# Kernel optimization log

Hardware: AMD Instinct MI355X
Metric: run time of the kernel (lower is better)

Reference implementation:

```python
import jax, jax.numpy as jnp
import numpy as np

N, E, EMB, EDGE, ITERS = 50000, 400000, 128, 32, 2
EPS = 1e-5


def setup_inputs() -> dict:
    key = jax.random.key(0)
    ks = jax.random.split(key, 8)
    s = 0.05

    def lin(k, i, o):
        return jax.random.normal(k, (i, o), jnp.float32) * s

    def mlp_params(k):
        k1, k2 = jax.random.split(k)
        return dict(W1=lin(k1, 2 * EMB + EDGE, EMB), b1=jnp.zeros((EMB,)),
                    g1=jnp.ones((EMB,)), be1=jnp.zeros((EMB,)),
                    W2=lin(k2, EMB, EMB), b2=jnp.zeros((EMB,)),
                    g2=jnp.ones((EMB,)), be2=jnp.zeros((EMB,)))

    p = mlp_params(ks[3])
    c = mlp_params(ks[4])
    inp = {
        'nodes': jax.random.normal(ks[0], (N, EMB), jnp.float32),
        'edges': jax.random.randint(ks[1], (2, E), 0, N, jnp.int64),
        'edge_attr': jax.random.normal(ks[2], (E, EDGE), jnp.float32),
        'fW': lin(ks[5], EMB, EMB), 'fb': jnp.zeros((EMB,)),
        'fg': jnp.ones((EMB,)), 'fbe': jnp.zeros((EMB,)),
    }
    for name, d in (('p', p), ('c', c)):
        for kk, v in d.items():
            inp[name + kk] = v
    return inp


def _bn(x, g, b):
    # training-mode BatchNorm1d: batch stats over axis 0, biased variance
    m = x.mean(0)
    v = x.var(0)
    return (x - m) * jax.lax.rsqrt(v + EPS) * g + b


def _edge_mlp(h, W1, b1, g1, be1, W2, b2, g2, be2):
    h = jax.nn.relu(_bn(h @ W1 + b1, g1, be1))
    return jax.nn.relu(_bn(h @ W2 + b2, g2, be2))


def _agg(x, idx_i, idx_j, ea, params):
    # message: mlp([x_i, x_j, edge_attr]); aggregate sum at idx_i; degree-normalize
    msg = _edge_mlp(jnp.concatenate([x[idx_i], x[idx_j], ea], axis=1), *params)
    summed = jax.ops.segment_sum(msg, idx_i, num_segments=x.shape[0])
    deg = jax.ops.segment_sum(jnp.ones(idx_i.shape, x.dtype), idx_i,
                              num_segments=x.shape[0])
    deg_inv = jnp.where(deg > 0, 1.0 / deg, 0.0)
    return summed * deg_inv[:, None]


def reference(nodes, edges, edge_attr,
              pW1, pb1, pg1, pbe1, pW2, pb2, pg2, pbe2,
              cW1, cb1, cg1, cbe1, cW2, cb2, cg2, cbe2,
              fW, fb, fg, fbe):
    src, dst = edges[0], edges[1]
    pp = (pW1, pb1, pg1, pbe1, pW2, pb2, pg2, pbe2)
    cp = (cW1, cb1, cg1, cbe1, cW2, cb2, cg2, cbe2)
    for _ in range(ITERS):
        fi = _agg(nodes, dst, src, edge_attr, pp)  # parent: source_to_target
        fo = _agg(nodes, src, dst, edge_attr, cp)  # child: target_to_source
        upd = jax.nn.relu(_bn((nodes + fi + fo) @ fW + fb, fg, fbe))
        nodes = nodes + upd
    return nodes
```

## Files before the change

kernel.cpp:

```cpp
#include <hip/hip_runtime.h>
#include <math.h>

#define NN 50000
#define EE 400000
#define EMBD 128
#define KIN 288
#define NITERS 2
#define EPSV 1e-5f
#define SAE 296
#define SA1 136
#define NT_E 6250
#define G0 1024
#define G1 1024

typedef __attribute__((ext_vector_type(8))) short bf16x8;
typedef __attribute__((ext_vector_type(4))) float f32x4;

#define MFMA16(a, b, c) __builtin_amdgcn_mfma_f32_16x16x32_bf16(a, b, c, 0, 0, 0)

__device__ __forceinline__ unsigned short f2bf(float x) {
  unsigned int u = __float_as_uint(x);
  u += 0x7fffu + ((u >> 16) & 1u);
  return (unsigned short)(u >> 16);
}

__device__ __forceinline__ int physch(int ch, int row) {
  return (ch < 32) ? ((ch & ~7) | ((ch ^ (row & 7)) & 7)) : ch;
}


__global__ void k_zeroi(int* __restrict__ p, int n) {
  for (int i = blockIdx.x * blockDim.x + threadIdx.x; i < n;
       i += gridDim.x * blockDim.x)
    p[i] = 0;
}

__global__ void k_detect(const long long* __restrict__ e64, int* __restrict__ flag) {
  __shared__ int ok;
  if (threadIdx.x == 0) ok = 1;
  __syncthreads();
  for (int i = threadIdx.x; i < 4096; i += blockDim.x) {
    const long long v = e64[i];
    if (v < 0 || v >= NN) atomicAnd(&ok, 0);
  }
  __syncthreads();
  if (threadIdx.x == 0) *flag = ok;
}

__global__ void k_convert(const void* __restrict__ edges, const int* __restrict__ flag,
                          int* __restrict__ src, int* __restrict__ dst) {
  const int is64 = *flag;
  for (int i = blockIdx.x * blockDim.x + threadIdx.x; i < 2 * EE;
       i += gridDim.x * blockDim.x) {
    const int v = is64 ? (int)((const long long*)edges)[i] : ((const int*)edges)[i];
    if (i < EE) src[i] = v; else dst[i - EE] = v;
  }
}

__global__ void k_count(const int* __restrict__ src, const int* __restrict__ dst,
                        int* __restrict__ degp, int* __restrict__ degc) {
  for (int e = blockIdx.x * blockDim.x + threadIdx.x; e < EE;
       e += gridDim.x * blockDim.x) {
    atomicAdd(&degp[dst[e]], 1);
    atomicAdd(&degc[src[e]], 1);
  }
}

__global__ void k_dinv(const int* __restrict__ dp, const int* __restrict__ dc,
                       float* __restrict__ ip, float* __restrict__ ic) {
  for (int n = blockIdx.x * blockDim.x + threadIdx.x; n < NN;
       n += gridDim.x * blockDim.x) {
    ip[n] = dp[n] ? 1.f / (float)dp[n] : 0.f;
    ic[n] = dc[n] ? 1.f / (float)dc[n] : 0.f;
  }
}

__global__ __launch_bounds__(1024) void k_scan(
    const int* __restrict__ degp, const int* __restrict__ degc,
    int* __restrict__ offp, int* __restrict__ offc) {
  const int* deg = blockIdx.x ? degc : degp;
  int* off = blockIdx.x ? offc : offp;
  __shared__ int sh[1024];
  const int t = threadIdx.x;
  int running = 0;
  for (int base = 0; base < NN; base += 1024) {
    const int v = (base + t < NN) ? deg[base + t] : 0;
    sh[t] = v;
    __syncthreads();
    for (int o = 1; o < 1024; o <<= 1) {
      const int y = (t >= o) ? sh[t - o] : 0;
      __syncthreads();
      sh[t] += y;
      __syncthreads();
    }
    if (base + t < NN) off[base + t] = running + sh[t] - v;
    running += sh[1023];
    __syncthreads();
  }
  if (t == 0) off[NN] = running;
}

__global__ void k_copycur(const int* __restrict__ offp, const int* __restrict__ offc,
                          int* __restrict__ curp, int* __restrict__ curc) {
  for (int i = blockIdx.x * blockDim.x + threadIdx.x; i < NN;
       i += gridDim.x * blockDim.x) {
    curp[i] = offp[i];
    curc[i] = offc[i];
  }
}

__global__ void k_scatter(const int* __restrict__ src, const int* __restrict__ dst,
                          int* __restrict__ curp, int* __restrict__ curc,
                          int* __restrict__ lstp, int* __restrict__ lstc) {
  for (int e = blockIdx.x * blockDim.x + threadIdx.x; e < EE;
       e += gridDim.x * blockDim.x) {
    const int pp = atomicAdd(&curp[dst[e]], 1);
    lstp[pp] = e;
    const int pc = atomicAdd(&curc[src[e]], 1);
    lstc[pc] = e;
  }
}

__global__ void k_initnodes(const float* __restrict__ in, float* __restrict__ nd,
                            unsigned short* __restrict__ xb) {
  const int tot = NN * EMBD / 4;
  for (int i = blockIdx.x * blockDim.x + threadIdx.x; i < tot;
       i += gridDim.x * blockDim.x) {
    const float4 v = ((const float4*)in)[i];
    ((float4*)nd)[i] = v;
    short4 b;
    b.x = (short)f2bf(v.x); b.y = (short)f2bf(v.y);
    b.z = (short)f2bf(v.z); b.w = (short)f2bf(v.w);
    *(short4*)&xb[(size_t)i * 4] = b;
  }
}

__global__ void k_prepW(const float* __restrict__ W, unsigned short* __restrict__ Wt,
                        int K) {
  const int idx = blockIdx.x * blockDim.x + threadIdx.x;
  if (idx < K * EMBD) {
    const int k = idx >> 7, n = idx & 127;
    Wt[(size_t)n * K + k] = f2bf(W[(size_t)k * EMBD + n]);
  }
}

__global__ void k_prepea(const float* __restrict__ ea,
                         unsigned short* __restrict__ eab) {
  const int tot = EE * 32 / 8;
  for (int i = blockIdx.x * blockDim.x + threadIdx.x; i < tot;
       i += gridDim.x * blockDim.x) {
    const float4 a = ((const float4*)ea)[i * 2];
    const float4 b = ((const float4*)ea)[i * 2 + 1];
    union { unsigned short u[8]; uint4 v; } o;
    o.u[0] = f2bf(a.x); o.u[1] = f2bf(a.y); o.u[2] = f2bf(a.z); o.u[3] = f2bf(a.w);
    o.u[4] = f2bf(b.x); o.u[5] = f2bf(b.y); o.u[6] = f2bf(b.z); o.u[7] = f2bf(b.w);
    ((uint4*)eab)[i] = o.v;
  }
}


template <int EAB>
__global__ __launch_bounds__(256, 1) void k_pass0(
    const unsigned short* __restrict__ xb, const int* __restrict__ idx_i,
    const int* __restrict__ idx_j, const float* __restrict__ ea,
    const unsigned short* __restrict__ eab,
    const unsigned short* __restrict__ W1t, float* __restrict__ stat,
    unsigned short* __restrict__ Y1) {
  __shared__ __align__(16) unsigned short Ab[64 * SAE];
  __shared__ float red[256];
  const int t = threadIdx.x;
  const int lane = t & 63, w = t >> 6, m = lane & 15, kg = lane >> 4;
  const int r = t >> 2, sub = t & 3;
  const int n0 = w * 32 + m, n1 = n0 + 16;
  bf16x8 B0[9], B1[9];
#pragma unroll
  for (int ks = 0; ks < 9; ++ks) {
    B0[ks] = *(const bf16x8*)&W1t[(size_t)n0 * KIN + ks * 32 + kg * 8];
    B1[ks] = *(const bf16x8*)&W1t[(size_t)n1 * KIN + ks * 32 + kg * 8];
  }
  float s0 = 0.f, s1 = 0.f, q0 = 0.f, q1 = 0.f;
  int tile = blockIdx.x;
  int inext = idx_i[tile * 64 + r];
  int jnext = idx_j[tile * 64 + r];
  while (tile < NT_E) {
    const int icur = inext, jcur = jnext;
    __syncthreads();
    {
      const uint4* xi = (const uint4*)(xb + (size_t)icur * EMBD);
      const uint4* xj = (const uint4*)(xb + (size_t)jcur * EMBD);
      unsigned short* rowp = &Ab[r * SAE];
#pragma unroll
      for (int qq = 0; qq < 8; ++qq) {
        const int c = sub + qq * 4;
        const uint4 v = (c < 16) ? xi[c] : xj[c - 16];
        *(uint4*)&rowp[physch(c, r) * 8] = v;
      }
      const int e = tile * 64 + r;
      uint4 ev;
      if (EAB) {
        ev = *(const uint4*)&eab[(size_t)e * 32 + sub * 8];
      } else {
        const float4 e0 = *(const float4*)&ea[(size_t)e * 32 + sub * 8];
        const float4 e1 = *(const float4*)&ea[(size_t)e * 32 + sub * 8 + 4];
        union { unsigned short u[8]; uint4 v4; } o;
        o.u[0] = f2bf(e0.x); o.u[1] = f2bf(e0.y); o.u[2] = f2bf(e0.z);
        o.u[3] = f2bf(e0.w); o.u[4] = f2bf(e1.x); o.u[5] = f2bf(e1.y);
        o.u[6] = f2bf(e1.z); o.u[7] = f2bf(e1.w);
        ev = o.v4;
      }
      *(uint4*)&rowp[(32 + sub) * 8] = ev;
    }
    __syncthreads();
    const int next = tile + gridDim.x;
    if (next < NT_E) {
      inext = idx_i[next * 64 + r];
      jnext = idx_j[next * 64 + r];
    }
    const f32x4 zz = {0.f, 0.f, 0.f, 0.f};
    f32x4 acc[4][2] = {{zz, zz}, {zz, zz}, {zz, zz}, {zz, zz}};
#pragma unroll
    for (int ks = 0; ks < 9; ++ks) {
      const int aoff = physch(ks * 4 + kg, m) * 8;
#pragma unroll
      for (int mt = 0; mt < 4; ++mt) {
        const bf16x8 a = *(const bf16x8*)&Ab[(mt * 16 + m) * SAE + aoff];
        acc[mt][0] = MFMA16(a, B0[ks], acc[mt][0]);
        acc[mt][1] = MFMA16(a, B1[ks], acc[mt][1]);
      }
    }
#pragma unroll
    for (int mt = 0; mt < 4; ++mt)
#pragma unroll
      for (int r2 = 0; r2 < 4; ++r2) {
        const float v0 = acc[mt][0][r2], v1 = acc[mt][1][r2];
        s0 += v0; q0 += v0 * v0;
        s1 += v1; q1 += v1 * v1;
      }
    __syncthreads();
#pragma unroll
    for (int nt = 0; nt < 2; ++nt) {
      const int c = w * 32 + nt * 16 + m;
      const int cc = c >> 3, cl = c & 7;
#pragma unroll
      for (int mt = 0; mt < 4; ++mt)
#pragma unroll
        for (int r2 = 0; r2 < 4; ++r2) {
          const int rw = mt * 16 + kg * 4 + r2;
          Ab[rw * SAE + physch(cc, rw) * 8 + cl] = f2bf(acc[mt][nt][r2]);
        }
    }
    __syncthreads();
    unsigned short* Yt = Y1 + (size_t)tile * 64 * EMBD;
#pragma unroll
    for (int i = 0; i < 4; ++i) {
      const int g = i * 2048 + t * 8;
      const int row = g >> 7, ch = (g >> 3) & 15;
      *(uint4*)&Yt[g] = *(const uint4*)&Ab[row * SAE + physch(ch, row) * 8];
    }
    tile = next;
  }
  s0 += __shfl_xor(s0, 16); s0 += __shfl_xor(s0, 32);
  q0 += __shfl_xor(q0, 16); q0 += __shfl_xor(q0, 32);
  s1 += __shfl_xor(s1, 16); s1 += __shfl_xor(s1, 32);
  q1 += __shfl_xor(q1, 16); q1 += __shfl_xor(q1, 32);
  if (kg == 0) {
    const int c0 = w * 32 + m, c1 = c0 + 16;
    red[c0] = s0; red[128 + c0] = q0;
    red[c1] = s1; red[128 + c1] = q1;
  }
  __syncthreads();
  if (t < 128) {
    atomicAdd(&stat[t], red[t]);
    atomicAdd(&stat[128 + t], red[128 + t]);
  }
}


__global__ __launch_bounds__(256, 3) void k_pass1(
    const unsigned short* __restrict__ W2t, float* __restrict__ stat,
    unsigned short* __restrict__ Y) {
  __shared__ __align__(16) unsigned short Ab[64 * SA1];
  __shared__ float red[256];
  const int t = threadIdx.x;
  const int lane = t & 63, w = t >> 6, m = lane & 15, kg = lane >> 4;
  const int n0 = w * 32 + m, n1 = n0 + 16;
  const int ch = t & 15;
  bf16x8 B0[4], B1[4];
#pragma unroll
  for (int ks = 0; ks < 4; ++ks) {
    B0[ks] = *(const bf16x8*)&W2t[(size_t)n0 * EMBD + ks * 32 + kg * 8];
    B1[ks] = *(const bf16x8*)&W2t[(size_t)n1 * EMBD + ks * 32 + kg * 8];
  }
  float scr[8], shr[8];
#pragma unroll
  for (int h = 0; h < 8; ++h) {
    scr[h] = stat[256 + ch * 8 + h];
    shr[h] = stat[384 + ch * 8 + h];
  }
  float s0 = 0.f, s1 = 0.f, q0 = 0.f, q1 = 0.f;
  uint4 yreg[4];
  int tile = blockIdx.x;
  {
    const unsigned short* Yt = Y + (size_t)tile * 64 * EMBD;
#pragma unroll
    for (int i = 0; i < 4; ++i)
      yreg[i] = *(const uint4*)&Yt[i * 2048 + t * 8];
  }
  while (tile < NT_E) {
    __syncthreads();
#pragma unroll
    for (int i = 0; i < 4; ++i) {
      const int row = i * 16 + (t >> 4);
      const unsigned int* pv = (const unsigned int*)&yreg[i];
      union { unsigned short u[8]; uint4 v; } o;
#pragma unroll
      for (int h = 0; h < 4; ++h) {
        const unsigned int pw = pv[h];
        const float f0 = __uint_as_float(pw << 16);
        const float f1 = __uint_as_float(pw & 0xffff0000u);
        o.u[h * 2] = f2bf(fmaxf(fmaf(f0, scr[h * 2], shr[h * 2]), 0.f));
        o.u[h * 2 + 1] = f2bf(fmaxf(fmaf(f1, scr[h * 2 + 1], shr[h * 2 + 1]), 0.f));
      }
      *(uint4*)&Ab[row * SA1 + physch(ch, row) * 8] = o.v;
    }
    __syncthreads();
    const int next = tile + gridDim.x;
    if (next < NT_E) {
      const unsigned short* Yt = Y + (size_t)next * 64 * EMBD;
#pragma unroll
      for (int i = 0; i < 4; ++i)
        yreg[i] = *(const uint4*)&Yt[i * 2048 + t * 8];
    }
    const f32x4 zz = {0.f, 0.f, 0.f, 0.f};
    f32x4 acc[4][2] = {{zz, zz}, {zz, zz}, {zz, zz}, {zz, zz}};
#pragma unroll
    for (int ks = 0; ks < 4; ++ks) {
      const int aoff = physch(ks * 4 + kg, m) * 8;
#pragma unroll
      for (int mt = 0; mt < 4; ++mt) {
        const bf16x8 a = *(const bf16x8*)&Ab[(mt * 16 + m) * SA1 + aoff];
        acc[mt][0] = MFMA16(a, B0[ks], acc[mt][0]);
        acc[mt][1] = MFMA16(a, B1[ks], acc[mt][1]);
      }
    }
#pragma unroll
    for (int mt = 0; mt < 4; ++mt)
#pragma unroll
      for (int r2 = 0; r2 < 4; ++r2) {
        const float v0 = acc[mt][0][r2], v1 = acc[mt][1][r2];
        s0 += v0; q0 += v0 * v0;
        s1 += v1; q1 += v1 * v1;
      }
    __syncthreads();
#pragma unroll
    for (int nt = 0; nt < 2; ++nt) {
      const int c = w * 32 + nt * 16 + m;
      const int cc = c >> 3, cl = c & 7;
#pragma unroll
      for (int mt = 0; mt < 4; ++mt)
#pragma unroll
        for (int r2 = 0; r2 < 4; ++r2) {
          const int rw = mt * 16 + kg * 4 + r2;
          Ab[rw * SA1 + physch(cc, rw) * 8 + cl] = f2bf(acc[mt][nt][r2]);
        }
    }
    __syncthreads();
    unsigned short* Yo = Y + (size_t)tile * 64 * EMBD;
#pragma unroll
    for (int i = 0; i < 4; ++i) {
      const int g = i * 2048 + t * 8;
      const int row = g >> 7, c2 = (g >> 3) & 15;
      *(uint4*)&Yo[g] = *(const uint4*)&Ab[row * SA1 + physch(c2, row) * 8];
    }
    tile = next;
  }
  s0 += __shfl_xor(s0, 16); s0 += __shfl_xor(s0, 32);
  q0 += __shfl_xor(q0, 16); q0 += __shfl_xor(q0, 32);
  s1 += __shfl_xor(s1, 16); s1 += __shfl_xor(s1, 32);
  q1 += __shfl_xor(q1, 16); q1 += __shfl_xor(q1, 32);
  if (kg == 0) {
    const int c0 = w * 32 + m, c1 = c0 + 16;
    red[c0] = s0; red[128 + c0] = q0;
    red[c1] = s1; red[128 + c1] = q1;
  }
  __syncthreads();
  if (t < 128) {
    atomicAdd(&stat[512 + t], red[t]);
    atomicAdd(&stat[640 + t], red[128 + t]);
  }
}


template <int ADD>
__global__ __launch_bounds__(256) void k_agg2(
    const unsigned short* __restrict__ Y2, const int* __restrict__ off,
    const int* __restrict__ lst, const float* __restrict__ stat,
    const float* __restrict__ dinv, float* __restrict__ agg) {
  const int n = blockIdx.x * 4 + (threadIdx.x >> 6);
  const int lane = threadIdx.x & 63;
  if (n >= NN) return;
  const int o0 = off[n], o1 = off[n + 1];
  const float sc0 = stat[768 + 2 * lane], sc1 = stat[768 + 2 * lane + 1];
  const float sh0 = stat[896 + 2 * lane], sh1 = stat[896 + 2 * lane + 1];
  float a0 = 0.f, a1 = 0.f;
  for (int o = o0; o < o1; ++o) {
    const int e = lst[o];
    const unsigned int pw = ((const unsigned int*)(Y2 + (size_t)e * EMBD))[lane];
    a0 += fmaxf(fmaf(__uint_as_float(pw << 16), sc0, sh0), 0.f);
    a1 += fmaxf(fmaf(__uint_as_float(pw & 0xffff0000u), sc1, sh1), 0.f);
  }
  const float d = dinv[n];
  float2 out;
  if (ADD) {
    const float2 prev = ((const float2*)(agg + (size_t)n * EMBD))[lane];
    out.x = prev.x + a0 * d;
    out.y = prev.y + a1 * d;
  } else {
    out.x = a0 * d;
    out.y = a1 * d;
  }
  ((float2*)(agg + (size_t)n * EMBD))[lane] = out;
}


template <int NK, bool SWZ>
__device__ __forceinline__ void gemm_g(const unsigned short* Ab, const int sa,
                                       const unsigned short* __restrict__ Wt,
                                       const int K, const int m, const int kg,
                                       const int w, f32x4 acc[4][2]) {
  const int n0 = w * 32 + m, n1 = n0 + 16;
#pragma unroll
  for (int ks = 0; ks < NK; ++ks) {
    const int koff = ks * 32 + kg * 8;
    const int aoff = SWZ ? physch(koff >> 3, m) * 8 : koff;
    const bf16x8 b0 = *(const bf16x8*)&Wt[(size_t)n0 * K + koff];
    const bf16x8 b1 = *(const bf16x8*)&Wt[(size_t)n1 * K + koff];
#pragma unroll
    for (int mt = 0; mt < 4; ++mt) {
      const bf16x8 a = *(const bf16x8*)&Ab[(mt * 16 + m) * sa + aoff];
      acc[mt][0] = MFMA16(a, b0, acc[mt][0]);
      acc[mt][1] = MFMA16(a, b1, acc[mt][1]);
    }
  }
}

__device__ __forceinline__ void stats_epi64(const f32x4 acc[4][2], float* red,
                                            float* __restrict__ statg, const int t,
                                            const int m, const int kg, const int w) {
#pragma unroll
  for (int nt = 0; nt < 2; ++nt) {
    float s = 0.f, q = 0.f;
#pragma unroll
    for (int mt = 0; mt < 4; ++mt)
#pragma unroll
      for (int r = 0; r < 4; ++r) {
        const float v = acc[mt][nt][r];
        s += v;
        q += v * v;
      }
    s += __shfl_xor(s, 16); s += __shfl_xor(s, 32);
    q += __shfl_xor(q, 16); q += __shfl_xor(q, 32);
    if (kg == 0) {
      const int c = w * 32 + nt * 16 + m;
      red[c] = s;
      red[128 + c] = q;
    }
  }
  __syncthreads();
  if (t < 128) {
    atomicAdd(&statg[t], red[t]);
    atomicAdd(&statg[128 + t], red[128 + t]);
  }
}

__global__ __launch_bounds__(256) void k_node(
    const float* __restrict__ nd, float* __restrict__ ag,
    const unsigned short* __restrict__ Wt, float* __restrict__ stat) {
  __shared__ __align__(16) unsigned short Ab[64 * SA1];
  __shared__ float red[256];
  const int t = threadIdx.x;
  const int n0 = blockIdx.x * 64;
  {
    const int r = t >> 2, sub = t & 3;
    const int row = n0 + r;
    unsigned short* drow = &Ab[r * SA1];
#pragma unroll
    for (int q = 0; q < 8; ++q) {
      const int c4 = sub + q * 4;
      float4 va;
      if (row < NN) {
        va = ((const float4*)(nd + (size_t)row * EMBD))[c4];
        const float4 vb = ((const float4*)(ag + (size_t)row * EMBD))[c4];
        va.x += vb.x; va.y += vb.y; va.z += vb.z; va.w += vb.w;
      } else {
        va.x = va.y = va.z = va.w = 0.f;
      }
      short4 b;
      b.x = (short)f2bf(va.x); b.y = (short)f2bf(va.y);
      b.z = (short)f2bf(va.z); b.w = (short)f2bf(va.w);
      *(short4*)&drow[c4 * 4] = b;
    }
  }
  __syncthreads();
  const int lane = t & 63, w = t >> 6, m = lane & 15, kg = lane >> 4;
  const f32x4 zz = {0.f, 0.f, 0.f, 0.f};
  f32x4 acc[4][2] = {{zz, zz}, {zz, zz}, {zz, zz}, {zz, zz}};
  gemm_g<4, false>(Ab, SA1, Wt, EMBD, m, kg, w, acc);
#pragma unroll
  for (int nt = 0; nt < 2; ++nt) {
    const int c = w * 32 + nt * 16 + m;
#pragma unroll
    for (int mt = 0; mt < 4; ++mt)
#pragma unroll
      for (int r = 0; r < 4; ++r) {
        const int row = n0 + mt * 16 + kg * 4 + r;
        if (row < NN) ag[(size_t)row * EMBD + c] = acc[mt][nt][r];
      }
  }
  stats_epi64(acc, red, stat, t, m, kg, w);
}


__global__ void k_finalize(float* __restrict__ statbase, const float* __restrict__ g,
                           const float* __restrict__ be, float cnt) {
  const int t = threadIdx.x;
  if (t < EMBD) {
    const float s = statbase[t], sq = statbase[EMBD + t];
    const float m = s / cnt;
    float v = sq / cnt - m * m;
    v = fmaxf(v, 0.f);
    const float rs = rsqrtf(v + EPSV);
    const float sc = g[t] * rs;
    statbase[256 + t] = sc;
    statbase[384 + t] = be[t] - m * sc;
    statbase[t] = 0.f;
    statbase[EMBD + t] = 0.f;
  }
}

__global__ void k_update(float* __restrict__ nd, unsigned short* __restrict__ xb,
                         const float* __restrict__ Z, const float* __restrict__ stat) {
  const float* sc = stat + 256;
  const float* sh = stat + 384;
  const int total = NN * EMBD / 4;
  for (int i = blockIdx.x * blockDim.x + threadIdx.x; i < total;
       i += gridDim.x * blockDim.x) {
    const int c4 = i & 31;
    const float4 v = ((const float4*)Z)[i];
    const float4 s4 = ((const float4*)sc)[c4];
    const float4 h4 = ((const float4*)sh)[c4];
    float4 nv = ((float4*)nd)[i];
    nv.x += fmaxf(fmaf(v.x, s4.x, h4.x), 0.f);
    nv.y += fmaxf(fmaf(v.y, s4.y, h4.y), 0.f);
    nv.z += fmaxf(fmaf(v.z, s4.z, h4.z), 0.f);
    nv.w += fmaxf(fmaf(v.w, s4.w, h4.w), 0.f);
    ((float4*)nd)[i] = nv;
    short4 b;
    b.x = (short)f2bf(nv.x); b.y = (short)f2bf(nv.y);
    b.z = (short)f2bf(nv.z); b.w = (short)f2bf(nv.w);
    *(short4*)&xb[(size_t)i * 4] = b;
  }
}


extern "C" void kernel_launch(void* const* d_in, const int* in_sizes, int n_in,
                              void* d_out, int out_size, void* d_ws, size_t ws_size,
                              hipStream_t stream) {
  const float* in_nodes = (const float*)d_in[0];
  const void* edges = d_in[1];
  const float* ea = (const float*)d_in[2];
  const float* fW = (const float*)d_in[3];
  const float* fg = (const float*)d_in[5];
  const float* fbe = (const float*)d_in[6];
  const float* p_[8];
  const float* c_[8];
  for (int i = 0; i < 8; ++i) {
    p_[i] = (const float*)d_in[7 + i];
    c_[i] = (const float*)d_in[15 + i];
  }
  float* nodes = (float*)d_out;

  char* base = (char*)d_ws;
  size_t cur = 0;
  auto take = [&](size_t bytes) -> void* {
    void* p = base + cur;
    cur = (cur + bytes + 255) & ~(size_t)255;
    return p;
  };
  float* agg = (float*)take((size_t)NN * EMBD * 4);
  unsigned short* xb = (unsigned short*)take((size_t)NN * EMBD * 2);
  int* src = (int*)take(EE * 4);
  int* dst = (int*)take(EE * 4);
  int* lstp = (int*)take(EE * 4);
  int* lstc = (int*)take(EE * 4);
  int* offp = (int*)take((NN + 1) * 4);
  int* offc = (int*)take((NN + 1) * 4);
  int* curp = (int*)take(NN * 4);
  int* curc = (int*)take(NN * 4);
  float* dinvp = (float*)take(NN * 4);
  float* dinvc = (float*)take(NN * 4);
  float* stat = (float*)take(1024 * 4);
  int* flag = (int*)take(4);
  unsigned short* pW1t = (unsigned short*)take((size_t)EMBD * KIN * 2);
  unsigned short* pW2t = (unsigned short*)take((size_t)EMBD * EMBD * 2);
  unsigned short* cW1t = (unsigned short*)take((size_t)EMBD * KIN * 2);
  unsigned short* cW2t = (unsigned short*)take((size_t)EMBD * EMBD * 2);
  unsigned short* fWt = (unsigned short*)take((size_t)EMBD * EMBD * 2);
  unsigned short* Y1 = (unsigned short*)take((size_t)EE * EMBD * 2);
  const size_t eab_bytes = (size_t)EE * 32 * 2;
  const bool useEab = (cur + eab_bytes) <= ws_size;
  unsigned short* eab = useEab ? (unsigned short*)take(eab_bytes) : nullptr;

  k_zeroi<<<64, 256, 0, stream>>>((int*)stat, 1024);
  k_zeroi<<<128, 256, 0, stream>>>(curp, NN);
  k_zeroi<<<128, 256, 0, stream>>>(curc, NN);
  k_detect<<<1, 256, 0, stream>>>((const long long*)edges, flag);
  k_convert<<<1024, 256, 0, stream>>>(edges, flag, src, dst);
  k_count<<<1024, 256, 0, stream>>>(src, dst, curp, curc);
  k_dinv<<<128, 256, 0, stream>>>(curp, curc, dinvp, dinvc);
  k_scan<<<2, 1024, 0, stream>>>(curp, curc, offp, offc);
  k_copycur<<<128, 256, 0, stream>>>(offp, offc, curp, curc);
  k_scatter<<<1024, 256, 0, stream>>>(src, dst, curp, curc, lstp, lstc);
  k_initnodes<<<2048, 256, 0, stream>>>(in_nodes, nodes, xb);
  k_prepW<<<(KIN * EMBD + 255) / 256, 256, 0, stream>>>(p_[0], pW1t, KIN);
  k_prepW<<<(EMBD * EMBD + 255) / 256, 256, 0, stream>>>(p_[4], pW2t, EMBD);
  k_prepW<<<(KIN * EMBD + 255) / 256, 256, 0, stream>>>(c_[0], cW1t, KIN);
  k_prepW<<<(EMBD * EMBD + 255) / 256, 256, 0, stream>>>(c_[4], cW2t, EMBD);
  k_prepW<<<(EMBD * EMBD + 255) / 256, 256, 0, stream>>>(fW, fWt, EMBD);
  if (useEab) k_prepea<<<2048, 256, 0, stream>>>(ea, eab);

  const int NB = (NN + 63) / 64;

  for (int it = 0; it < NITERS; ++it) {
    if (useEab)
      k_pass0<1><<<G0, 256, 0, stream>>>(xb, dst, src, ea, eab, pW1t, stat, Y1);
    else
      k_pass0<0><<<G0, 256, 0, stream>>>(xb, dst, src, ea, eab, pW1t, stat, Y1);
    k_finalize<<<1, 128, 0, stream>>>(stat, p_[2], p_[3], (float)EE);
    k_pass1<<<G1, 256, 0, stream>>>(pW2t, stat, Y1);
    k_finalize<<<1, 128, 0, stream>>>(stat + 512, p_[6], p_[7], (float)EE);
    k_agg2<0><<<NN / 4, 256, 0, stream>>>(Y1, offp, lstp, stat, dinvp, agg);
    if (useEab)
      k_pass0<1><<<G0, 256, 0, stream>>>(xb, src, dst, ea, eab, cW1t, stat, Y1);
    else
      k_pass0<0><<<G0, 256, 0, stream>>>(xb, src, dst, ea, eab, cW1t, stat, Y1);
    k_finalize<<<1, 128, 0, stream>>>(stat, c_[2], c_[3], (float)EE);
    k_pass1<<<G1, 256, 0, stream>>>(cW2t, stat, Y1);
    k_finalize<<<1, 128, 0, stream>>>(stat + 512, c_[6], c_[7], (float)EE);
    k_agg2<1><<<NN / 4, 256, 0, stream>>>(Y1, offc, lstc, stat, dinvc, agg);
    k_node<<<NB, 256, 0, stream>>>(nodes, agg, fWt, stat);
    k_finalize<<<1, 128, 0, stream>>>(stat, fg, fbe, (float)NN);
    k_update<<<2048, 256, 0, stream>>>(nodes, xb, agg, stat);
  }
}
```

Before: 1.061 ms.

## Fuse parent and child first-layer edge GEMMs into one pass sharing gathered inputs

Adds a fused pass0 kernel that gathers [x_dst, x_src, ea] once per edge tile and computes both the parent and child first-layer GEMMs. The child weights are pre-permuted by swapping the first two 128-row K blocks, so the same gathered tile serves the reversed concatenation. This halves the random node gathers and tile staging, at the cost of a second edge-sized intermediate buffer, twice the resident weight registers and separate stat buffers. It also replaces the serial chunked degree scan with a per-thread-chunk scan using a single block-level prefix pass.

```diff
diff --git a/kernel.cpp b/kernel.cpp
--- a/kernel.cpp
+++ b/kernel.cpp
@@ -75,29 +75,38 @@
   }
 }
 
-__global__ __launch_bounds__(1024) void k_scan(
+__global__ __launch_bounds__(1024) void k_scan2(
     const int* __restrict__ degp, const int* __restrict__ degc,
     int* __restrict__ offp, int* __restrict__ offc) {
   const int* deg = blockIdx.x ? degc : degp;
   int* off = blockIdx.x ? offc : offp;
   __shared__ int sh[1024];
   const int t = threadIdx.x;
-  int running = 0;
-  for (int base = 0; base < NN; base += 1024) {
-    const int v = (base + t < NN) ? deg[base + t] : 0;
-    sh[t] = v;
-    __syncthreads();
-    for (int o = 1; o < 1024; o <<= 1) {
-      const int y = (t >= o) ? sh[t - o] : 0;
-      __syncthreads();
-      sh[t] += y;
-      __syncthreads();
-    }
-    if (base + t < NN) off[base + t] = running + sh[t] - v;
-    running += sh[1023];
-    __syncthreads();
-  }
-  if (t == 0) off[NN] = running;
+  const int i0 = t * 49;
+  int s = 0;
+#pragma unroll 1
+  for (int k = 0; k < 49; ++k) {
+    const int i = i0 + k;
+    if (i < NN) s += deg[i];
+  }
+  sh[t] = s;
+  __syncthreads();
+  for (int o = 1; o < 1024; o <<= 1) {
+    const int y = (t >= o) ? sh[t - o] : 0;
+    __syncthreads();
+    sh[t] += y;
+    __syncthreads();
+  }
+  int base = sh[t] - s;
+#pragma unroll 1
+  for (int k = 0; k < 49; ++k) {
+    const int i = i0 + k;
+    if (i < NN) {
+      off[i] = base;
+      base += deg[i];
+    }
+  }
+  if (t == 1023) off[NN] = sh[1023];
 }
 
 __global__ void k_copycur(const int* __restrict__ offp, const int* __restrict__ offc,
@@ -136,11 +145,12 @@
 }
 
 __global__ void k_prepW(const float* __restrict__ W, unsigned short* __restrict__ Wt,
-                        int K) {
+                        int K, int swap) {
   const int idx = blockIdx.x * blockDim.x + threadIdx.x;
   if (idx < K * EMBD) {
     const int k = idx >> 7, n = idx & 127;
-    Wt[(size_t)n * K + k] = f2bf(W[(size_t)k * EMBD + n]);
+    const int ksw = (swap && k < 256) ? (k ^ 128) : k;
+    Wt[(size_t)n * K + ksw] = f2bf(W[(size_t)k * EMBD + n]);
   }
 }
 
@@ -155,6 +165,142 @@
     o.u[0] = f2bf(a.x); o.u[1] = f2bf(a.y); o.u[2] = f2bf(a.z); o.u[3] = f2bf(a.w);
     o.u[4] = f2bf(b.x); o.u[5] = f2bf(b.y); o.u[6] = f2bf(b.z); o.u[7] = f2bf(b.w);
     ((uint4*)eab)[i] = o.v;
+  }
+}
+
+
+template <int EAB>
+__global__ __launch_bounds__(256, 1) void k_pass0f(
+    const unsigned short* __restrict__ xb, const int* __restrict__ idx_i,
+    const int* __restrict__ idx_j, const float* __restrict__ ea,
+    const unsigned short* __restrict__ eab,
+    const unsigned short* __restrict__ Wp, const unsigned short* __restrict__ Wc,
+    float* __restrict__ statP, float* __restrict__ statC,
+    unsigned short* __restrict__ Yp, unsigned short* __restrict__ Yc) {
+  __shared__ __align__(16) unsigned short Ab[64 * SAE];
+  __shared__ float red[512];
+  const int t = threadIdx.x;
+  const int lane = t & 63, w = t >> 6, m = lane & 15, kg = lane >> 4;
+  const int r = t >> 2, sub = t & 3;
+  const int n0 = w * 32 + m, n1 = n0 + 16;
+  bf16x8 Bp0[9], Bp1[9], Bc0[9], Bc1[9];
+#pragma unroll
+  for (int ks = 0; ks < 9; ++ks) {
+    Bp0[ks] = *(const bf16x8*)&Wp[(size_t)n0 * KIN + ks * 32 + kg * 8];
+    Bp1[ks] = *(const bf16x8*)&Wp[(size_t)n1 * KIN + ks * 32 + kg * 8];
+    Bc0[ks] = *(const bf16x8*)&Wc[(size_t)n0 * KIN + ks * 32 + kg * 8];
+    Bc1[ks] = *(const bf16x8*)&Wc[(size_t)n1 * KIN + ks * 32 + kg * 8];
+  }
+  float ps0 = 0.f, ps1 = 0.f, pq0 = 0.f, pq1 = 0.f;
+  float cs0 = 0.f, cs1 = 0.f, cq0 = 0.f, cq1 = 0.f;
+  int tile = blockIdx.x;
+  int inext = idx_i[tile * 64 + r];
+  int jnext = idx_j[tile * 64 + r];
+  while (tile < NT_E) {
+    const int icur = inext, jcur = jnext;
+    __syncthreads();
+    {
+      const uint4* xi = (const uint4*)(xb + (size_t)icur * EMBD);
+      const uint4* xj = (const uint4*)(xb + (size_t)jcur * EMBD);
+      unsigned short* rowp = &Ab[r * SAE];
+#pragma unroll
+      for (int qq = 0; qq < 8; ++qq) {
+        const int c = sub + qq * 4;
+        const uint4 v = (c < 16) ? xi[c] : xj[c - 16];
+        *(uint4*)&rowp[physch(c, r) * 8] = v;
+      }
+      const int e = tile * 64 + r;
+      uint4 ev;
+      if (EAB) {
+        ev = *(const uint4*)&eab[(size_t)e * 32 + sub * 8];
+      } else {
+        const float4 e0 = *(const float4*)&ea[(size_t)e * 32 + sub * 8];
+        const float4 e1 = *(const float4*)&ea[(size_t)e * 32 + sub * 8 + 4];
+        union { unsigned short u[8]; uint4 v4; } o;
+        o.u[0] = f2bf(e0.x); o.u[1] = f2bf(e0.y); o.u[2] = f2bf(e0.z);
+        o.u[3] = f2bf(e0.w); o.u[4] = f2bf(e1.x); o.u[5] = f2bf(e1.y);
+        o.u[6] = f2bf(e1.z); o.u[7] = f2bf(e1.w);
+        ev = o.v4;
+      }
+      *(uint4*)&rowp[(32 + sub) * 8] = ev;
+    }
+    __syncthreads();
+    const int next = tile + gridDim.x;
+    if (next < NT_E) {
+      inext = idx_i[next * 64 + r];
+      jnext = idx_j[next * 64 + r];
+    }
+    const f32x4 zz = {0.f, 0.f, 0.f, 0.f};
+    f32x4 ap[4][2] = {{zz, zz}, {zz, zz}, {zz, zz}, {zz, zz}};
+    f32x4 ac[4][2] = {{zz, zz}, {zz, zz}, {zz, zz}, {zz, zz}};
+#pragma unroll
+    for (int ks = 0; ks < 9; ++ks) {
+      const int aoff = physch(ks * 4 + kg, m) * 8;
+#pragma unroll
+      for (int mt = 0; mt < 4; ++mt) {
+        const bf16x8 a = *(const bf16x8*)&Ab[(mt * 16 + m) * SAE + aoff];
+        ap[mt][0] = MFMA16(a, Bp0[ks], ap[mt][0]);
+        ap[mt][1] = MFMA16(a, Bp1[ks], ap[mt][1]);
+        ac[mt][0] = MFMA16(a, Bc0[ks], ac[mt][0]);
+        ac[mt][1] = MFMA16(a, Bc1[ks], ac[mt][1]);
+      }
+    }
+#pragma unroll
+    for (int mt = 0; mt < 4; ++mt)
+#pragma unroll
+      for (int r2 = 0; r2 < 4; ++r2) {
+        const float p0 = ap[mt][0][r2], p1 = ap[mt][1][r2];
+        ps0 += p0; pq0 += p0 * p0; ps1 += p1; pq1 += p1 * p1;
+        const float c0 = ac[mt][0][r2], c1 = ac[mt][1][r2];
+        cs0 += c0; cq0 += c0 * c0; cs1 += c1; cq1 += c1 * c1;
+      }
+    __syncthreads();
+#pragma unroll
+    for (int nt = 0; nt < 2; ++nt) {
+      const int c = w * 32 + nt * 16 + m;
+      const int cc = c >> 3, cl = c & 7;
+#pragma unroll
+      for (int mt = 0; mt < 4; ++mt)
+#pragma unroll
+        for (int r2 = 0; r2 < 4; ++r2) {
+          const int rw = mt * 16 + kg * 4 + r2;
+          Ab[rw * SAE + physch(cc, rw) * 8 + cl] = f2bf(ap[mt][nt][r2]);
+          Ab[rw * SAE + physch(16 + cc, rw) * 8 + cl] = f2bf(ac[mt][nt][r2]);
+        }
+    }
+    __syncthreads();
+    unsigned short* Ytp = Yp + (size_t)tile * 64 * EMBD;
+    unsigned short* Ytc = Yc + (size_t)tile * 64 * EMBD;
+#pragma unroll
+    for (int i = 0; i < 4; ++i) {
+      const int g = i * 2048 + t * 8;
+      const int row = g >> 7, ch = (g >> 3) & 15;
+      *(uint4*)&Ytp[g] = *(const uint4*)&Ab[row * SAE + physch(ch, row) * 8];
+      *(uint4*)&Ytc[g] = *(const uint4*)&Ab[row * SAE + physch(ch + 16, row) * 8];
+    }
+    tile = next;
+  }
+  ps0 += __shfl_xor(ps0, 16); ps0 += __shfl_xor(ps0, 32);
+  pq0 += __shfl_xor(pq0, 16); pq0 += __shfl_xor(pq0, 32);
+  ps1 += __shfl_xor(ps1, 16); ps1 += __shfl_xor(ps1, 32);
+  pq1 += __shfl_xor(pq1, 16); pq1 += __shfl_xor(pq1, 32);
+  cs0 += __shfl_xor(cs0, 16); cs0 += __shfl_xor(cs0, 32);
+  cq0 += __shfl_xor(cq0, 16); cq0 += __shfl_xor(cq0, 32);
+  cs1 += __shfl_xor(cs1, 16); cs1 += __shfl_xor(cs1, 32);
+  cq1 += __shfl_xor(cq1, 16); cq1 += __shfl_xor(cq1, 32);
+  if (kg == 0) {
+    const int c0 = w * 32 + m, c1 = c0 + 16;
+    red[c0] = ps0; red[128 + c0] = pq0;
+    red[c1] = ps1; red[128 + c1] = pq1;
+    red[256 + c0] = cs0; red[384 + c0] = cq0;
+    red[256 + c1] = cs1; red[384 + c1] = cq1;
+  }
+  __syncthreads();
+  if (t < 128) {
+    atomicAdd(&statP[t], red[t]);
+    atomicAdd(&statP[128 + t], red[128 + t]);
+    atomicAdd(&statC[t], red[256 + t]);
+    atomicAdd(&statC[128 + t], red[384 + t]);
   }
 }
 
@@ -599,57 +745,81 @@
   int* curc = (int*)take(NN * 4);
   float* dinvp = (float*)take(NN * 4);
   float* dinvc = (float*)take(NN * 4);
-  float* stat = (float*)take(1024 * 4);
+  float* stat = (float*)take(2048 * 4);
   int* flag = (int*)take(4);
   unsigned short* pW1t = (unsigned short*)take((size_t)EMBD * KIN * 2);
   unsigned short* pW2t = (unsigned short*)take((size_t)EMBD * EMBD * 2);
   unsigned short* cW1t = (unsigned short*)take((size_t)EMBD * KIN * 2);
+  unsigned short* cW1ts = (unsigned short*)take((size_t)EMBD * KIN * 2);
   unsigned short* cW2t = (unsigned short*)take((size_t)EMBD * EMBD * 2);
   unsigned short* fWt = (unsigned short*)take((size_t)EMBD * EMBD * 2);
-  unsigned short* Y1 = (unsigned short*)take((size_t)EE * EMBD * 2);
+  unsigned short* Y1p = (unsigned short*)take((size_t)EE * EMBD * 2);
+  const size_t y_bytes = (size_t)EE * EMBD * 2;
+  const bool useF = (cur + y_bytes) <= ws_size;
+  unsigned short* Y1c = useF ? (unsigned short*)take(y_bytes) : nullptr;
   const size_t eab_bytes = (size_t)EE * 32 * 2;
   const bool useEab = (cur + eab_bytes) <= ws_size;
   unsigned short* eab = useEab ? (unsigned short*)take(eab_bytes) : nullptr;
 
-  k_zeroi<<<64, 256, 0, stream>>>((int*)stat, 1024);
+  k_zeroi<<<64, 256, 0, stream>>>((int*)stat, 2048);
   k_zeroi<<<128, 256, 0, stream>>>(curp, NN);
   k_zeroi<<<128, 256, 0, stream>>>(curc, NN);
   k_detect<<<1, 256, 0, stream>>>((const long long*)edges, flag);
   k_convert<<<1024, 256, 0, stream>>>(edges, flag, src, dst);
   k_count<<<1024, 256, 0, stream>>>(src, dst, curp, curc);
   k_dinv<<<128, 256, 0, stream>>>(curp, curc, dinvp, dinvc);
-  k_scan<<<2, 1024, 0, stream>>>(curp, curc, offp, offc);
+  k_scan2<<<2, 1024, 0, stream>>>(curp, curc, offp, offc);
   k_copycur<<<128, 256, 0, stream>>>(offp, offc, curp, curc);
   k_scatter<<<1024, 256, 0, stream>>>(src, dst, curp, curc, lstp, lstc);
   k_initnodes<<<2048, 256, 0, stream>>>(in_nodes, nodes, xb);
-  k_prepW<<<(KIN * EMBD + 255) / 256, 256, 0, stream>>>(p_[0], pW1t, KIN);
-  k_prepW<<<(EMBD * EMBD + 255) / 256, 256, 0, stream>>>(p_[4], pW2t, EMBD);
-  k_prepW<<<(KIN * EMBD + 255) / 256, 256, 0, stream>>>(c_[0], cW1t, KIN);
-  k_prepW<<<(EMBD * EMBD + 255) / 256, 256, 0, stream>>>(c_[4], cW2t, EMBD);
-  k_prepW<<<(EMBD * EMBD + 255) / 256, 256, 0, stream>>>(fW, fWt, EMBD);
+  k_prepW<<<(KIN * EMBD + 255) / 256, 256, 0, stream>>>(p_[0], pW1t, KIN, 0);
+  k_prepW<<<(EMBD * EMBD + 255) / 256, 256, 0, stream>>>(p_[4], pW2t, EMBD, 0);
+  k_prepW<<<(KIN * EMBD + 255) / 256, 256, 0, stream>>>(c_[0], cW1t, KIN, 0);
+  k_prepW<<<(KIN * EMBD + 255) / 256, 256, 0, stream>>>(c_[0], cW1ts, KIN, 1);
+  k_prepW<<<(EMBD * EMBD + 255) / 256, 256, 0, stream>>>(c_[4], cW2t, EMBD, 0);
+  k_prepW<<<(EMBD * EMBD + 255) / 256, 256, 0, stream>>>(fW, fWt, EMBD, 0);
   if (useEab) k_prepea<<<2048, 256, 0, stream>>>(ea, eab);
 
   const int NB = (NN + 63) / 64;
+  float* statP = stat;
+  float* statC = stat + 1024;
 
   for (int it = 0; it < NITERS; ++it) {
-    if (useEab)
-      k_pass0<1><<<G0, 256, 0, stream>>>(xb, dst, src, ea, eab, pW1t, stat, Y1);
-    else
-      k_pass0<0><<<G0, 256, 0, stream>>>(xb, dst, src, ea, eab, pW1t, stat, Y1);
-    k_finalize<<<1, 128, 0, stream>>>(stat, p_[2], p_[3], (float)EE);
-    k_pass1<<<G1, 256, 0, stream>>>(pW2t, stat, Y1);
-    k_finalize<<<1, 128, 0, stream>>>(stat + 512, p_[6], p_[7], (float)EE);
-    k_agg2<0><<<NN / 4, 256, 0, stream>>>(Y1, offp, lstp, stat, dinvp, agg);
-    if (useEab)
-      k_pass0<1><<<G0, 256, 0, stream>>>(xb, src, dst, ea, eab, cW1t, stat, Y1);
-    else
-      k_pass0<0><<<G0, 256, 0, stream>>>(xb, src, dst, ea, eab, cW1t, stat, Y1);
-    k_finalize<<<1, 128, 0, stream>>>(stat, c_[2], c_[3], (float)EE);
-    k_pass1<<<G1, 256, 0, stream>>>(cW2t, stat, Y1);
-    k_finalize<<<1, 128, 0, stream>>>(stat + 512, c_[6], c_[7], (float)EE);
-    k_agg2<1><<<NN / 4, 256, 0, stream>>>(Y1, offc, lstc, stat, dinvc, agg);
-    k_node<<<NB, 256, 0, stream>>>(nodes, agg, fWt, stat);
-    k_finalize<<<1, 128, 0, stream>>>(stat, fg, fbe, (float)NN);
-    k_update<<<2048, 256, 0, stream>>>(nodes, xb, agg, stat);
-  }
-}
+    if (useF) {
+      if (useEab)
+        k_pass0f<1><<<G0, 256, 0, stream>>>(xb, dst, src, ea, eab, pW1t, cW1ts,
+                                            statP, statC, Y1p, Y1c);
+      else
+        k_pass0f<0><<<G0, 256, 0, stream>>>(xb, dst, src, ea, eab, pW1t, cW1ts,
+                                            statP, statC, Y1p, Y1c);
+      k_finalize<<<1, 128, 0, stream>>>(statP, p_[2], p_[3], (float)EE);
+      k_finalize<<<1, 128, 0, stream>>>(statC, c_[2], c_[3], (float)EE);
+      k_pass1<<<G1, 256, 0, stream>>>(pW2t, statP, Y1p);
+      k_finalize<<<1, 128, 0, stream>>>(statP + 512, p_[6], p_[7], (float)EE);
+      k_agg2<0><<<NN / 4, 256, 0, stream>>>(Y1p, offp, lstp, statP, dinvp, agg);
+      k_pass1<<<G1, 256, 0, stream>>>(cW2t, statC, Y1c);
+      k_finalize<<<1, 128, 0, stream>>>(statC + 512, c_[6], c_[7], (float)EE);
+      k_agg2<1><<<NN / 4, 256, 0, stream>>>(Y1c, offc, lstc, statC, dinvc, agg);
+    } else {
+      if (useEab)
+        k_pass0<1><<<G0, 256, 0, stream>>>(xb, dst, src, ea, eab, pW1t, statP, Y1p);
+      else
+        k_pass0<0><<<G0, 256, 0, stream>>>(xb, dst, src, ea, eab, pW1t, statP, Y1p);
+      k_finalize<<<1, 128, 0, stream>>>(statP, p_[2], p_[3], (float)EE);
+      k_pass1<<<G1, 256, 0, stream>>>(pW2t, statP, Y1p);
+      k_finalize<<<1, 128, 0, stream>>>(statP + 512, p_[6], p_[7], (float)EE);
+      k_agg2<0><<<NN / 4, 256, 0, stream>>>(Y1p, offp, lstp, statP, dinvp, agg);
+      if (useEab)
+        k_pass0<1><<<G0, 256, 0, stream>>>(xb, src, dst, ea, eab, cW1t, statP, Y1p);
+      else
+        k_pass0<0><<<G0, 256, 0, stream>>>(xb, src, dst, ea, eab, cW1t, statP, Y1p);
+      k_finalize<<<1, 128, 0, stream>>>(statP, c_[2], c_[3], (float)EE);
+      k_pass1<<<G1, 256, 0, stream>>>(cW2t, statP, Y1p);
+      k_finalize<<<1, 128, 0, stream>>>(statP + 512, c_[6], c_[7], (float)EE);
+      k_agg2<1><<<NN / 4, 256, 0, stream>>>(Y1p, offc, lstc, statP, dinvc, agg);
+    }
+    k_node<<<NB, 256, 0, stream>>>(nodes, agg, fWt, statP);
+    k_finalize<<<1, 128, 0, stream>>>(statP, fg, fbe, (float)NN);
+    k_update<<<2048, 256, 0, stream>>>(nodes, xb, agg, statP);
+  }
+}
```

After: 1.107 ms. +4.4%, slower.

## Merge parent and child message passes into single launches with separate buffers

Applied to the files above, without the earlier changes.

Runs the parent and child edge-MLP passes concurrently by launching combined kernels whose first half of blocks handles the parent direction and the second half the child direction, each with its own Y buffer and stats. Aggregation for both directions is fused into one kernel, and BN finalize runs both in one launch. The degree scan is rewritten as a per-thread chunked sum plus a single block scan instead of repeated 1024-element scans. This cuts kernel launch count and serialization and fills the GPU with more blocks, at the cost of a second 100MB intermediate buffer and more memory traffic pressure.

```diff
diff --git a/kernel.cpp b/kernel.cpp
--- a/kernel.cpp
+++ b/kernel.cpp
@@ -10,7 +10,7 @@
 #define SAE 296
 #define SA1 136
 #define NT_E 6250
-#define G0 1024
+#define G0P 1024
 #define G1 1024
 
 typedef __attribute__((ext_vector_type(8))) short bf16x8;
@@ -75,29 +75,38 @@
   }
 }
 
-__global__ __launch_bounds__(1024) void k_scan(
+__global__ __launch_bounds__(1024) void k_scan2(
     const int* __restrict__ degp, const int* __restrict__ degc,
     int* __restrict__ offp, int* __restrict__ offc) {
   const int* deg = blockIdx.x ? degc : degp;
   int* off = blockIdx.x ? offc : offp;
   __shared__ int sh[1024];
   const int t = threadIdx.x;
-  int running = 0;
-  for (int base = 0; base < NN; base += 1024) {
-    const int v = (base + t < NN) ? deg[base + t] : 0;
-    sh[t] = v;
-    __syncthreads();
-    for (int o = 1; o < 1024; o <<= 1) {
-      const int y = (t >= o) ? sh[t - o] : 0;
-      __syncthreads();
-      sh[t] += y;
-      __syncthreads();
-    }
-    if (base + t < NN) off[base + t] = running + sh[t] - v;
-    running += sh[1023];
-    __syncthreads();
-  }
-  if (t == 0) off[NN] = running;
+  const int i0 = t * 49;
+  int s = 0;
+#pragma unroll 1
+  for (int k = 0; k < 49; ++k) {
+    const int i = i0 + k;
+    if (i < NN) s += deg[i];
+  }
+  sh[t] = s;
+  __syncthreads();
+  for (int o = 1; o < 1024; o <<= 1) {
+    const int y = (t >= o) ? sh[t - o] : 0;
+    __syncthreads();
+    sh[t] += y;
+    __syncthreads();
+  }
+  int base = sh[t] - s;
+#pragma unroll 1
+  for (int k = 0; k < 49; ++k) {
+    const int i = i0 + k;
+    if (i < NN) {
+      off[i] = base;
+      base += deg[i];
+    }
+  }
+  if (t == 1023) off[NN] = sh[1023];
 }
 
 __global__ void k_copycur(const int* __restrict__ offp, const int* __restrict__ offc,
@@ -160,14 +169,25 @@
 
 
 template <int EAB>
-__global__ __launch_bounds__(256, 1) void k_pass0(
-    const unsigned short* __restrict__ xb, const int* __restrict__ idx_i,
-    const int* __restrict__ idx_j, const float* __restrict__ ea,
-    const unsigned short* __restrict__ eab,
-    const unsigned short* __restrict__ W1t, float* __restrict__ stat,
-    unsigned short* __restrict__ Y1) {
+__global__ __launch_bounds__(256, 1) void k_pass0m(
+    const unsigned short* __restrict__ xb,
+    const int* __restrict__ i0, const int* __restrict__ j0,
+    const unsigned short* __restrict__ W0, float* __restrict__ st0,
+    unsigned short* __restrict__ Y0,
+    const int* __restrict__ i1, const int* __restrict__ j1,
+    const unsigned short* __restrict__ W1, float* __restrict__ st1,
+    unsigned short* __restrict__ Y1,
+    const float* __restrict__ ea, const unsigned short* __restrict__ eab,
+    const int nb0) {
   __shared__ __align__(16) unsigned short Ab[64 * SAE];
   __shared__ float red[256];
+  const int phase = (blockIdx.x >= nb0) ? 1 : 0;
+  const int* __restrict__ idx_i = phase ? i1 : i0;
+  const int* __restrict__ idx_j = phase ? j1 : j0;
+  const unsigned short* __restrict__ W1t = phase ? W1 : W0;
+  float* __restrict__ stat = phase ? st1 : st0;
+  unsigned short* __restrict__ Y = phase ? Y1 : Y0;
+  const int stride = phase ? ((int)gridDim.x - nb0) : nb0;
   const int t = threadIdx.x;
   const int lane = t & 63, w = t >> 6, m = lane & 15, kg = lane >> 4;
   const int r = t >> 2, sub = t & 3;
@@ -179,7 +199,7 @@
     B1[ks] = *(const bf16x8*)&W1t[(size_t)n1 * KIN + ks * 32 + kg * 8];
   }
   float s0 = 0.f, s1 = 0.f, q0 = 0.f, q1 = 0.f;
-  int tile = blockIdx.x;
+  int tile = blockIdx.x - phase * nb0;
   int inext = idx_i[tile * 64 + r];
   int jnext = idx_j[tile * 64 + r];
   while (tile < NT_E) {
@@ -211,7 +231,7 @@
       *(uint4*)&rowp[(32 + sub) * 8] = ev;
     }
     __syncthreads();
-    const int next = tile + gridDim.x;
+    const int next = tile + stride;
     if (next < NT_E) {
       inext = idx_i[next * 64 + r];
       jnext = idx_j[next * 64 + r];
@@ -250,7 +270,7 @@
         }
     }
     __syncthreads();
-    unsigned short* Yt = Y1 + (size_t)tile * 64 * EMBD;
+    unsigned short* Yt = Y + (size_t)tile * 64 * EMBD;
 #pragma unroll
     for (int i = 0; i < 4; ++i) {
       const int g = i * 2048 + t * 8;
@@ -276,9 +296,9 @@
 }
 
 
-__global__ __launch_bounds__(256, 3) void k_pass1(
+__device__ __forceinline__ void pass1_body(
     const unsigned short* __restrict__ W2t, float* __restrict__ stat,
-    unsigned short* __restrict__ Y) {
+    unsigned short* __restrict__ Y, int tile, const int stride) {
   __shared__ __align__(16) unsigned short Ab[64 * SA1];
   __shared__ float red[256];
   const int t = threadIdx.x;
@@ -299,7 +319,6 @@
   }
   float s0 = 0.f, s1 = 0.f, q0 = 0.f, q1 = 0.f;
   uint4 yreg[4];
-  int tile = blockIdx.x;
   {
     const unsigned short* Yt = Y + (size_t)tile * 64 * EMBD;
 #pragma unroll
@@ -324,7 +343,7 @@
       *(uint4*)&Ab[row * SA1 + physch(ch, row) * 8] = o.v;
     }
     __syncthreads();
-    const int next = tile + gridDim.x;
+    const int next = tile + stride;
     if (next < NT_E) {
       const unsigned short* Yt = Y + (size_t)next * 64 * EMBD;
 #pragma unroll
@@ -390,6 +409,70 @@
   }
 }
 
+__global__ __launch_bounds__(256, 3) void k_pass1(
+    const unsigned short* __restrict__ W2t, float* __restrict__ stat,
+    unsigned short* __restrict__ Y) {
+  pass1_body(W2t, stat, Y, blockIdx.x, G1);
+}
+
+__global__ __launch_bounds__(256, 3) void k_pass1m(
+    const unsigned short* __restrict__ Wp, const unsigned short* __restrict__ Wc,
+    float* __restrict__ statP, float* __restrict__ statC,
+    unsigned short* __restrict__ Yp, unsigned short* __restrict__ Yc) {
+  const int phase = (blockIdx.x >= G1) ? 1 : 0;
+  const unsigned short* W2t = phase ? Wc : Wp;
+  float* stat = phase ? statC : statP;
+  unsigned short* Y = phase ? Yc : Yp;
+  pass1_body(W2t, stat, Y, blockIdx.x - phase * G1, G1);
+}
+
+
+__global__ __launch_bounds__(256) void k_aggm(
+    const unsigned short* __restrict__ Yp, const unsigned short* __restrict__ Yc,
+    const int* __restrict__ offp, const int* __restrict__ lstp,
+    const int* __restrict__ offc, const int* __restrict__ lstc,
+    const float* __restrict__ statP, const float* __restrict__ statC,
+    const float* __restrict__ dinvp, const float* __restrict__ dinvc,
+    float* __restrict__ agg) {
+  const int n = blockIdx.x * 4 + (threadIdx.x >> 6);
+  const int lane = threadIdx.x & 63;
+  if (n >= NN) return;
+  float r0, r1;
+  {
+    const int o0 = offp[n], o1 = offp[n + 1];
+    const float sc0 = statP[768 + 2 * lane], sc1 = statP[768 + 2 * lane + 1];
+    const float sh0 = statP[896 + 2 * lane], sh1 = statP[896 + 2 * lane + 1];
+    float a0 = 0.f, a1 = 0.f;
+    for (int o = o0; o < o1; ++o) {
+      const int e = lstp[o];
+      const unsigned int pw = ((const unsigned int*)(Yp + (size_t)e * EMBD))[lane];
+      a0 += fmaxf(fmaf(__uint_as_float(pw << 16), sc0, sh0), 0.f);
+      a1 += fmaxf(fmaf(__uint_as_float(pw & 0xffff0000u), sc1, sh1), 0.f);
+    }
+    const float d = dinvp[n];
+    r0 = a0 * d;
+    r1 = a1 * d;
+  }
+  {
+    const int o0 = offc[n], o1 = offc[n + 1];
+    const float sc0 = statC[768 + 2 * lane], sc1 = statC[768 + 2 * lane + 1];
+    const float sh0 = statC[896 + 2 * lane], sh1 = statC[896 + 2 * lane + 1];
+    float a0 = 0.f, a1 = 0.f;
+    for (int o = o0; o < o1; ++o) {
+      const int e = lstc[o];
+      const unsigned int pw = ((const unsigned int*)(Yc + (size_t)e * EMBD))[lane];
+      a0 += fmaxf(fmaf(__uint_as_float(pw << 16), sc0, sh0), 0.f);
+      a1 += fmaxf(fmaf(__uint_as_float(pw & 0xffff0000u), sc1, sh1), 0.f);
+    }
+    const float d = dinvc[n];
+    r0 += a0 * d;
+    r1 += a1 * d;
+  }
+  float2 out;
+  out.x = r0;
+  out.y = r1;
+  ((float2*)(agg + (size_t)n * EMBD))[lane] = out;
+}
 
 template <int ADD>
 __global__ __launch_bounds__(256) void k_agg2(
@@ -521,21 +604,35 @@
 }
 
 
+__device__ __forceinline__ void finalize_one(float* __restrict__ sb,
+                                             const float* __restrict__ g,
+                                             const float* __restrict__ be,
+                                             float cnt, int c) {
+  const float s = sb[c], sq = sb[EMBD + c];
+  const float m = s / cnt;
+  float v = sq / cnt - m * m;
+  v = fmaxf(v, 0.f);
+  const float rs = rsqrtf(v + EPSV);
+  const float sc = g[c] * rs;
+  sb[256 + c] = sc;
+  sb[384 + c] = be[c] - m * sc;
+  sb[c] = 0.f;
+  sb[EMBD + c] = 0.f;
+}
+
 __global__ void k_finalize(float* __restrict__ statbase, const float* __restrict__ g,
                            const float* __restrict__ be, float cnt) {
   const int t = threadIdx.x;
-  if (t < EMBD) {
-    const float s = statbase[t], sq = statbase[EMBD + t];
-    const float m = s / cnt;
-    float v = sq / cnt - m * m;
-    v = fmaxf(v, 0.f);
-    const float rs = rsqrtf(v + EPSV);
-    const float sc = g[t] * rs;
-    statbase[256 + t] = sc;
-    statbase[384 + t] = be[t] - m * sc;
-    statbase[t] = 0.f;
-    statbase[EMBD + t] = 0.f;
-  }
+  if (t < EMBD) finalize_one(statbase, g, be, cnt, t);
+}
+
+__global__ void k_finalize2(float* __restrict__ sA, const float* __restrict__ gA,
+                            const float* __restrict__ bA, float* __restrict__ sB,
+                            const float* __restrict__ gB, const float* __restrict__ bB,
+                            float cnt) {
+  const int t = threadIdx.x;
+  if (t < EMBD) finalize_one(sA, gA, bA, cnt, t);
+  else finalize_one(sB, gB, bB, cnt, t - EMBD);
 }
 
 __global__ void k_update(float* __restrict__ nd, unsigned short* __restrict__ xb,
@@ -599,26 +696,29 @@
   int* curc = (int*)take(NN * 4);
   float* dinvp = (float*)take(NN * 4);
   float* dinvc = (float*)take(NN * 4);
-  float* stat = (float*)take(1024 * 4);
+  float* stat = (float*)take(2048 * 4);
   int* flag = (int*)take(4);
   unsigned short* pW1t = (unsigned short*)take((size_t)EMBD * KIN * 2);
   unsigned short* pW2t = (unsigned short*)take((size_t)EMBD * EMBD * 2);
   unsigned short* cW1t = (unsigned short*)take((size_t)EMBD * KIN * 2);
   unsigned short* cW2t = (unsigned short*)take((size_t)EMBD * EMBD * 2);
   unsigned short* fWt = (unsigned short*)take((size_t)EMBD * EMBD * 2);
-  unsigned short* Y1 = (unsigned short*)take((size_t)EE * EMBD * 2);
+  unsigned short* Y1p = (unsigned short*)take((size_t)EE * EMBD * 2);
+  const size_t y_bytes = (size_t)EE * EMBD * 2;
+  const bool useM = (cur + y_bytes) <= ws_size;
+  unsigned short* Y1c = useM ? (unsigned short*)take(y_bytes) : nullptr;
   const size_t eab_bytes = (size_t)EE * 32 * 2;
   const bool useEab = (cur + eab_bytes) <= ws_size;
   unsigned short* eab = useEab ? (unsigned short*)take(eab_bytes) : nullptr;
 
-  k_zeroi<<<64, 256, 0, stream>>>((int*)stat, 1024);
+  k_zeroi<<<64, 256, 0, stream>>>((int*)stat, 2048);
   k_zeroi<<<128, 256, 0, stream>>>(curp, NN);
   k_zeroi<<<128, 256, 0, stream>>>(curc, NN);
   k_detect<<<1, 256, 0, stream>>>((const long long*)edges, flag);
   k_convert<<<1024, 256, 0, stream>>>(edges, flag, src, dst);
   k_count<<<1024, 256, 0, stream>>>(src, dst, curp, curc);
   k_dinv<<<128, 256, 0, stream>>>(curp, curc, dinvp, dinvc);
-  k_scan<<<2, 1024, 0, stream>>>(curp, curc, offp, offc);
+  k_scan2<<<2, 1024, 0, stream>>>(curp, curc, offp, offc);
   k_copycur<<<128, 256, 0, stream>>>(offp, offc, curp, curc);
   k_scatter<<<1024, 256, 0, stream>>>(src, dst, curp, curc, lstp, lstc);
   k_initnodes<<<2048, 256, 0, stream>>>(in_nodes, nodes, xb);
@@ -630,26 +730,54 @@
   if (useEab) k_prepea<<<2048, 256, 0, stream>>>(ea, eab);
 
   const int NB = (NN + 63) / 64;
+  float* statP = stat;
+  float* statC = stat + 1024;
 
   for (int it = 0; it < NITERS; ++it) {
-    if (useEab)
-      k_pass0<1><<<G0, 256, 0, stream>>>(xb, dst, src, ea, eab, pW1t, stat, Y1);
-    else
-      k_pass0<0><<<G0, 256, 0, stream>>>(xb, dst, src, ea, eab, pW1t, stat, Y1);
-    k_finalize<<<1, 128, 0, stream>>>(stat, p_[2], p_[3], (float)EE);
-    k_pass1<<<G1, 256, 0, stream>>>(pW2t, stat, Y1);
-    k_finalize<<<1, 128, 0, stream>>>(stat + 512, p_[6], p_[7], (float)EE);
-    k_agg2<0><<<NN / 4, 256, 0, stream>>>(Y1, offp, lstp, stat, dinvp, agg);
-    if (useEab)
-      k_pass0<1><<<G0, 256, 0, stream>>>(xb, src, dst, ea, eab, cW1t, stat, Y1);
-    else
-      k_pass0<0><<<G0, 256, 0, stream>>>(xb, src, dst, ea, eab, cW1t, stat, Y1);
-    k_finalize<<<1, 128, 0, stream>>>(stat, c_[2], c_[3], (float)EE);
-    k_pass1<<<G1, 256, 0, stream>>>(cW2t, stat, Y1);
-    k_finalize<<<1, 128, 0, stream>>>(stat + 512, c_[6], c_[7], (float)EE);
-    k_agg2<1><<<NN / 4, 256, 0, stream>>>(Y1, offc, lstc, stat, dinvc, agg);
-    k_node<<<NB, 256, 0, stream>>>(nodes, agg, fWt, stat);
-    k_finalize<<<1, 128, 0, stream>>>(stat, fg, fbe, (float)NN);
-    k_update<<<2048, 256, 0, stream>>>(nodes, xb, agg, stat);
-  }
-}
+    if (useM) {
+      if (useEab)
+        k_pass0m<1><<<2 * G0P, 256, 0, stream>>>(
+            xb, dst, src, pW1t, statP, Y1p, src, dst, cW1t, statC, Y1c,
+            ea, eab, G0P);
+      else
+        k_pass0m<0><<<2 * G0P, 256, 0, stream>>>(
+            xb, dst, src, pW1t, statP, Y1p, src, dst, cW1t, statC, Y1c,
+            ea, eab, G0P);
+      k_finalize2<<<1, 256, 0, stream>>>(statP, p_[2], p_[3],
+                                         statC, c_[2], c_[3], (float)EE);
+      k_pass1m<<<2 * G1, 256, 0, stream>>>(pW2t, cW2t, statP, statC, Y1p, Y1c);
+      k_finalize2<<<1, 256, 0, stream>>>(statP + 512, p_[6], p_[7],
+                                         statC + 512, c_[6], c_[7], (float)EE);
+      k_aggm<<<NN / 4, 256, 0, stream>>>(Y1p, Y1c, offp, lstp, offc, lstc,
+                                         statP, statC, dinvp, dinvc, agg);
+    } else {
+      if (useEab)
+        k_pass0m<1><<<G0P, 256, 0, stream>>>(
+            xb, dst, src, pW1t, statP, Y1p, dst, src, pW1t, statP, Y1p,
+            ea, eab, G0P);
+      else
+        k_pass0m<0><<<G0P, 256, 0, stream>>>(
+            xb, dst, src, pW1t, statP, Y1p, dst, src, pW1t, statP, Y1p,
+            ea, eab, G0P);
+      k_finalize<<<1, 128, 0, stream>>>(statP, p_[2], p_[3], (float)EE);
+      k_pass1<<<G1, 256, 0, stream>>>(pW2t, statP, Y1p);
+      k_finalize<<<1, 128, 0, stream>>>(statP + 512, p_[6], p_[7], (float)EE);
+      k_agg2<0><<<NN / 4, 256, 0, stream>>>(Y1p, offp, lstp, statP, dinvp, agg);
+      if (useEab)
+        k_pass0m<1><<<G0P, 256, 0, stream>>>(
+            xb, src, dst, cW1t, statP, Y1p, src, dst, cW1t, statP, Y1p,
+            ea, eab, G0P);
+      else
+        k_pass0m<0><<<G0P, 256, 0, stream>>>(
+            xb, src, dst, cW1t, statP, Y1p, src, dst, cW1t, statP, Y1p,
+            ea, eab, G0P);
+      k_finalize<<<1, 128, 0, stream>>>(statP, c_[2], c_[3], (float)EE);
+      k_pass1<<<G1, 256, 0, stream>>>(cW2t, statP, Y1p);
+      k_finalize<<<1, 128, 0, stream>>>(statP + 512, c_[6], c_[7], (float)EE);
+      k_agg2<1><<<NN / 4, 256, 0, stream>>>(Y1p, offc, lstc, statP, dinvc, agg);
+    }
+    k_node<<<NB, 256, 0, stream>>>(nodes, agg, fWt, statP);
+    k_finalize<<<1, 128, 0, stream>>>(statP, fg, fbe, (float)NN);
+    k_update<<<2048, 256, 0, stream>>>(nodes, xb, agg, statP);
+  }
+}
```

After: 986.5 us. -7.0%, faster.
